# Optimization experiments

Measured on AMD Instinct MI355X. Metric: run time of the kernel, lower is better.

Reference implementation:

```python
import jax, jax.numpy as jnp
import numpy as np
import math

N = 100000   # outputSize (memory bank rows)
D = 128      # inputSize (feature dim)
B = 128      # batch size
K = 4096     # number of negatives per sample
T = 0.07     # temperature
MOMENTUM = 0.5


def setup_inputs() -> dict:
    key = jax.random.key(0)
    k1, k2, k3, k4, k5 = jax.random.split(key, 5)
    stdv = 1.0 / math.sqrt(D / 3.0)
    # l2-normalized features, as produced by the encoder in contrastive setups
    v1 = jax.random.normal(k1, (B, D), dtype=jnp.float32)
    v1 = v1 / jnp.linalg.norm(v1, axis=1, keepdims=True)
    v2 = jax.random.normal(k2, (B, D), dtype=jnp.float32)
    v2 = v2 / jnp.linalg.norm(v2, axis=1, keepdims=True)
    idx = jax.random.randint(k3, (B, K + 1), 0, N, dtype=jnp.int32)  # pos+neg bank rows
    y = jnp.arange(B, dtype=jnp.int32)  # distinct positive slots (first-visit behavior)
    # memory buffers initialized U(-stdv, stdv), as in torch.rand*2*stdv - stdv
    memory_v1 = jax.random.uniform(k4, (N, D), dtype=jnp.float32, minval=-stdv, maxval=stdv)
    memory_v2 = jax.random.uniform(k5, (N, D), dtype=jnp.float32, minval=-stdv, maxval=stdv)
    return {"v1": v1, "v2": v2, "idx": idx, "y": y,
            "memory_v1": memory_v1, "memory_v2": memory_v2}


def reference(v1, v2, idx, y, memory_v1, memory_v2):
    n_out = memory_v1.shape[0]
    # gather K+1 rows per sample (detached in the original -> stop_gradient)
    w1 = jax.lax.stop_gradient(memory_v1[idx])  # [B, K+1, D]
    w2 = jax.lax.stop_gradient(memory_v2[idx])  # [B, K+1, D]
    # batched vector-matrix product + exp/T
    out_v2 = jnp.exp(jnp.einsum('bkd,bd->bk', w1, v2) / T)  # [B, K+1]
    out_v1 = jnp.exp(jnp.einsum('bkd,bd->bk', w2, v1) / T)  # [B, K+1]
    # normalization constants (first-call Z computation: mean * outputSize)
    Z_v1 = jax.lax.stop_gradient(out_v1.mean()) * n_out
    Z_v2 = jax.lax.stop_gradient(out_v2.mean()) * n_out
    out_v1 = out_v1 / Z_v1
    out_v2 = out_v2 / Z_v2
    # momentum-blended normalize-and-scatter memory update (no_grad in torch)
    upd1 = MOMENTUM * memory_v1[y] + (1.0 - MOMENTUM) * v1  # [B, D]
    upd1 = upd1 / jnp.linalg.norm(upd1, axis=1, keepdims=True)
    new_memory_v1 = memory_v1.at[y].set(upd1)
    upd2 = MOMENTUM * memory_v2[y] + (1.0 - MOMENTUM) * v2
    upd2 = upd2 / jnp.linalg.norm(upd2, axis=1, keepdims=True)
    new_memory_v2 = memory_v2.at[y].set(upd2)
    return out_v1, out_v2, new_memory_v1, new_memory_v2
```

## Files before the change

### kernel.cpp

```cpp
#include <hip/hip_runtime.h>
#include <math.h>

constexpr int N_ROWS = 100000;
constexpr int D      = 128;
constexpr int B      = 128;
constexpr int KP1    = 4097;
constexpr int TOTAL_PAIRS = B * KP1;
constexpr float INV_T = 1.0f / 0.07f;
constexpr int N4 = N_ROWS * (D / 4);

constexpr int RPB  = 40;
constexpr int NB   = N_ROWS / RPB;
constexpr int PADR = 33;

constexpr size_t WS_BCNT   = 64;
constexpr size_t WS_BSTART = WS_BCNT + (size_t)NB * 16 * 4;
constexpr size_t WS_PLIST  = WS_BSTART + (size_t)(NB + 4) * 4;
constexpr size_t WS_NEEDED = WS_PLIST + (size_t)TOTAL_PAIRS * 4;
constexpr size_t WS_ZERO_BYTES = WS_BSTART;

typedef float fvec4 __attribute__((ext_vector_type(4)));

__device__ __forceinline__ float dot4(float4 a, float4 b) {
    return a.x * b.x + a.y * b.y + a.z * b.z + a.w * b.w;
}
__device__ __forceinline__ float red32(float v) {
    #pragma unroll
    for (int off = 16; off >= 1; off >>= 1) v += __shfl_xor(v, off);
    return v;
}

__global__ __launch_bounds__(256) void hist_kernel(
    const int* __restrict__ idx, int* __restrict__ bcnt) {
    int stride = gridDim.x * 256;
    for (int p = blockIdx.x * 256 + threadIdx.x; p < TOTAL_PAIRS; p += stride) {
        int bkt = idx[p] / RPB;
        atomicAdd(&bcnt[bkt * 16], 1);
    }
}

__global__ __launch_bounds__(1024) void scan_kernel(
    int* __restrict__ bcnt, int* __restrict__ bstart) {
    __shared__ int ssum[1024];
    const int t = threadIdx.x;
    const int b0 = 3 * t;
    int c0 = (b0     < NB) ? bcnt[(b0    ) * 16] : 0;
    int c1 = (b0 + 1 < NB) ? bcnt[(b0 + 1) * 16] : 0;
    int c2 = (b0 + 2 < NB) ? bcnt[(b0 + 2) * 16] : 0;
    int local = c0 + c1 + c2;
    ssum[t] = local;
    __syncthreads();
    for (int off = 1; off < 1024; off <<= 1) {
        int v = (t >= off) ? ssum[t - off] : 0;
        __syncthreads();
        ssum[t] += v;
        __syncthreads();
    }
    int excl = ssum[t] - local;
    if (b0     < NB) { bstart[b0]     = excl;           bcnt[(b0    ) * 16] = excl; }
    if (b0 + 1 < NB) { bstart[b0 + 1] = excl + c0;      bcnt[(b0 + 1) * 16] = excl + c0; }
    if (b0 + 2 < NB) { bstart[b0 + 2] = excl + c0 + c1; bcnt[(b0 + 2) * 16] = excl + c0 + c1; }
    if (t == 1023) bstart[NB] = ssum[1023];
}

__global__ __launch_bounds__(256) void scatter_kernel(
    const int* __restrict__ idx, int* __restrict__ bcnt,
    unsigned* __restrict__ plist) {
    int stride = gridDim.x * 256;
    for (int p = blockIdx.x * 256 + threadIdx.x; p < TOTAL_PAIRS; p += stride) {
        int r   = idx[p];
        int bkt = r / RPB;
        int lr  = r - bkt * RPB;
        int pos = atomicAdd(&bcnt[bkt * 16], 1);
        plist[pos] = (unsigned)p | ((unsigned)lr << 20);
    }
}

__global__ __launch_bounds__(256) void fused_kernel(
    const float* __restrict__ v1, const float* __restrict__ v2,
    const float* __restrict__ mem1, const float* __restrict__ mem2,
    const int* __restrict__ bstart, const unsigned* __restrict__ plist,
    float* __restrict__ out, float* __restrict__ sums,
    float* __restrict__ o1, float* __restrict__ o2)
{
    __shared__ float4 sm1[RPB * PADR];
    __shared__ float4 sm2[RPB * PADR];
    __shared__ float sz1[4], sz2[4];

    const int bid = blockIdx.x;
    const int tid = threadIdx.x;
    const int r0  = bid * RPB;

    const float4* __restrict__ M1 = (const float4*)mem1;
    const float4* __restrict__ M2 = (const float4*)mem2;
    const float4* __restrict__ V1 = (const float4*)v1;
    const float4* __restrict__ V2 = (const float4*)v2;
    fvec4* __restrict__ d1 = (fvec4*)o1;
    fvec4* __restrict__ d2 = (fvec4*)o2;

    for (int i = tid; i < RPB * 32; i += 256) {
        int lr = i >> 5, c = i & 31;
        size_t gi = (size_t)(r0 + lr) * 32 + c;
        float4 x1 = M1[gi];
        float4 x2 = M2[gi];
        sm1[lr * PADR + c] = x1;
        sm2[lr * PADR + c] = x2;
        fvec4 y1 = {x1.x, x1.y, x1.z, x1.w};
        fvec4 y2 = {x2.x, x2.y, x2.z, x2.w};
        __builtin_nontemporal_store(y1, &d1[gi]);
        __builtin_nontemporal_store(y2, &d2[gi]);
    }
    __syncthreads();

    const int team = tid >> 3;
    const int sub  = tid & 7;
    const int qend = bstart[bid + 1];
    float az1 = 0.0f, az2 = 0.0f;

    for (int q = bstart[bid] + team; q < qend; q += 32) {
        unsigned v = plist[q];
        int p  = (int)(v & 0xFFFFFu);
        int lr = (int)(v >> 20);
        int b  = p / KP1;

        const float4* __restrict__ w1 = &sm1[lr * PADR];
        const float4* __restrict__ w2 = &sm2[lr * PADR];
        float a = 0.0f, bb = 0.0f;
        #pragma unroll
        for (int i = 0; i < 4; ++i) {
            int c = sub + 8 * i;
            float4 vv1 = V1[b * 32 + c];
            float4 vv2 = V2[b * 32 + c];
            float4 x2  = w2[c];
            float4 x1  = w1[c];
            a  += dot4(x2, vv1);
            bb += dot4(x1, vv2);
        }
        #pragma unroll
        for (int off = 4; off >= 1; off >>= 1) {
            a  += __shfl_xor(a,  off);
            bb += __shfl_xor(bb, off);
        }
        float eA = __expf(a  * INV_T);
        float eB = __expf(bb * INV_T);
        az1 += eA;
        az2 += eB;
        if (sub < 2) out[(sub ? TOTAL_PAIRS : 0) + p] = sub ? eB : eA;
    }

    #pragma unroll
    for (int off = 32; off >= 1; off >>= 1) {
        az1 += __shfl_xor(az1, off);
        az2 += __shfl_xor(az2, off);
    }
    if ((tid & 63) == 0) { sz1[tid >> 6] = az1; sz2[tid >> 6] = az2; }
    __syncthreads();
    if (tid == 0) {
        float t1 = (sz1[0] + sz1[1] + sz1[2] + sz1[3]) * 0.125f;
        float t2 = (sz2[0] + sz2[1] + sz2[2] + sz2[3]) * 0.125f;
        atomicAdd(&sums[0], t1);
        atomicAdd(&sums[1], t2);
    }
}

__global__ __launch_bounds__(256) void finish_kernel(
    float* __restrict__ out, const float* __restrict__ sums,
    const float* __restrict__ v1, const float* __restrict__ v2,
    const int* __restrict__ y,
    const float* __restrict__ mem1, const float* __restrict__ mem2,
    float* __restrict__ o1, float* __restrict__ o2)
{
    if (blockIdx.x < 2 * B && threadIdx.x < 64) {
        int b    = blockIdx.x & (B - 1);
        int bank = blockIdx.x >> 7;
        int lane = threadIdx.x;
        const float2* __restrict__ m = (const float2*)(bank ? mem2 : mem1);
        const float2* __restrict__ v = (const float2*)(bank ? v2 : v1);
        float2* __restrict__ o       = (float2*)(bank ? o2 : o1);
        int row = y[b];
        float2 mv = m[(size_t)row * 64 + lane];
        float2 vv = v[b * 64 + lane];
        float2 u;
        u.x = 0.5f * mv.x + 0.5f * vv.x;
        u.y = 0.5f * mv.y + 0.5f * vv.y;
        float ss = u.x * u.x + u.y * u.y;
        #pragma unroll
        for (int off = 32; off >= 1; off >>= 1) ss += __shfl_xor(ss, off);
        float inv = 1.0f / sqrtf(ss);
        float2 r; r.x = u.x * inv; r.y = u.y * inv;
        o[(size_t)row * 64 + lane] = r;
    }

    float sc1 = (float)((double)TOTAL_PAIRS / ((double)sums[0] * (double)N_ROWS));
    float sc2 = (float)((double)TOTAL_PAIRS / ((double)sums[1] * (double)N_ROWS));
    int stride = gridDim.x * blockDim.x;
    for (int i = blockIdx.x * blockDim.x + threadIdx.x; i < 2 * TOTAL_PAIRS;
         i += stride) {
        out[i] *= (i < TOTAL_PAIRS) ? sc1 : sc2;
    }
}

__global__ void init_ws_kernel(float* ws) {
    if (threadIdx.x < 2) ws[threadIdx.x] = 0.0f;
}

__global__ __launch_bounds__(256) void score_kernel(
    const float* __restrict__ v1, const float* __restrict__ v2,
    const int* __restrict__ idx,
    const float* __restrict__ mem1, const float* __restrict__ mem2,
    float* __restrict__ out, float* __restrict__ sums)
{
    __shared__ alignas(16) int s_idx[260];
    __shared__ float s1[8], s2[8];
    const int sid   = blockIdx.x;
    const int tid   = threadIdx.x;
    const int l     = tid & 31;
    const int grp   = tid >> 5;
    const int b     = sid >> 4;
    const int chunk = sid & 15;
    const int cnt   = (chunk == 15) ? 257 : 256;
    const int ibase = b * KP1 + chunk * 256;
    for (int t = tid; t < cnt; t += 256) s_idx[t] = idx[ibase + t];
    __syncthreads();
    const float4* __restrict__ m1 = (const float4*)mem1;
    const float4* __restrict__ m2 = (const float4*)mem2;
    const float4 a1 = ((const float4*)v1)[b * 32 + l];
    const float4 a2 = ((const float4*)v2)[b * 32 + l];
    const int lk = grp * 32, pbase = ibase + lk;
    float acc1 = 0.0f, acc2 = 0.0f;
    for (int u = 0; u < 32; u += 4) {
        const int4 rr = *(const int4*)&s_idx[lk + u];
        float4 wA0 = m2[(size_t)rr.x * 32 + l], wB0 = m1[(size_t)rr.x * 32 + l];
        float4 wA1 = m2[(size_t)rr.y * 32 + l], wB1 = m1[(size_t)rr.y * 32 + l];
        float4 wA2 = m2[(size_t)rr.z * 32 + l], wB2 = m1[(size_t)rr.z * 32 + l];
        float4 wA3 = m2[(size_t)rr.w * 32 + l], wB3 = m1[(size_t)rr.w * 32 + l];
        float eA0 = __expf(red32(dot4(wA0, a1)) * INV_T);
        float eB0 = __expf(red32(dot4(wB0, a2)) * INV_T);
        float eA1 = __expf(red32(dot4(wA1, a1)) * INV_T);
        float eB1 = __expf(red32(dot4(wB1, a2)) * INV_T);
        float eA2 = __expf(red32(dot4(wA2, a1)) * INV_T);
        float eB2 = __expf(red32(dot4(wB2, a2)) * INV_T);
        float eA3 = __expf(red32(dot4(wA3, a1)) * INV_T);
        float eB3 = __expf(red32(dot4(wB3, a2)) * INV_T);
        acc1 += (eA0 + eA1) + (eA2 + eA3);
        acc2 += (eB0 + eB1) + (eB2 + eB3);
        float sa = (l & 1) ? eA1 : eA0, sb = (l & 1) ? eA3 : eA2;
        float evA = (l & 2) ? sb : sa;
        float sc = (l & 1) ? eB1 : eB0, sd = (l & 1) ? eB3 : eB2;
        float evB = (l & 2) ? sd : sc;
        int p = pbase + u;
        if (l < 4)      out[p + l] = evA;
        else if (l < 8) out[TOTAL_PAIRS + p + (l - 4)] = evB;
    }
    if (chunk == 15 && grp == 7) {
        int r = s_idx[256];
        float4 wA = m2[(size_t)r * 32 + l], wB = m1[(size_t)r * 32 + l];
        float eA = __expf(red32(dot4(wA, a1)) * INV_T);
        float eB = __expf(red32(dot4(wB, a2)) * INV_T);
        acc1 += eA; acc2 += eB;
        if (l == 0) {
            out[b * KP1 + 4096] = eA;
            out[TOTAL_PAIRS + b * KP1 + 4096] = eB;
        }
    }
    if (l == 0) { s1[grp] = acc1; s2[grp] = acc2; }
    __syncthreads();
    if (tid == 0) {
        float t1 = 0.0f, t2 = 0.0f;
        #pragma unroll
        for (int i = 0; i < 8; ++i) { t1 += s1[i]; t2 += s2[i]; }
        atomicAdd(&sums[0], t1);
        atomicAdd(&sums[1], t2);
    }
}

__global__ __launch_bounds__(256) void copy_scale_kernel(
    const float* __restrict__ mem1, const float* __restrict__ mem2,
    float* __restrict__ o1, float* __restrict__ o2,
    float* __restrict__ out, const float* __restrict__ sums)
{
    const fvec4* __restrict__ m1 = (const fvec4*)mem1;
    const fvec4* __restrict__ m2 = (const fvec4*)mem2;
    fvec4* __restrict__ d1 = (fvec4*)o1;
    fvec4* __restrict__ d2 = (fvec4*)o2;
    int tid = blockIdx.x * 256 + threadIdx.x;
    int stride = gridDim.x * 256;
    for (int i = tid; i < N4; i += stride) {
        fvec4 x1 = m1[i], x2 = m2[i];
        __builtin_nontemporal_store(x1, &d1[i]);
        __builtin_nontemporal_store(x2, &d2[i]);
    }
    float sc1 = (float)((double)TOTAL_PAIRS / ((double)sums[0] * (double)N_ROWS));
    float sc2 = (float)((double)TOTAL_PAIRS / ((double)sums[1] * (double)N_ROWS));
    for (int i = tid; i < 2 * TOTAL_PAIRS; i += stride) {
        out[i] *= (i < TOTAL_PAIRS) ? sc1 : sc2;
    }
}

__global__ void rowupd_kernel(
    const float* __restrict__ v1, const float* __restrict__ v2,
    const int* __restrict__ y,
    const float* __restrict__ mem1, const float* __restrict__ mem2,
    float* __restrict__ o1, float* __restrict__ o2)
{
    int b    = blockIdx.x & (B - 1);
    int bank = blockIdx.x >> 7;
    int lane = threadIdx.x;
    const float2* __restrict__ m = (const float2*)(bank ? mem2 : mem1);
    const float2* __restrict__ v = (const float2*)(bank ? v2 : v1);
    float2* __restrict__ o       = (float2*)(bank ? o2 : o1);
    int row = y[b];
    float2 mv = m[(size_t)row * 64 + lane];
    float2 vv = v[b * 64 + lane];
    float2 u;
    u.x = 0.5f * mv.x + 0.5f * vv.x;
    u.y = 0.5f * mv.y + 0.5f * vv.y;
    float ss = u.x * u.x + u.y * u.y;
    #pragma unroll
    for (int off = 32; off >= 1; off >>= 1) ss += __shfl_xor(ss, off);
    float inv = 1.0f / sqrtf(ss);
    float2 r; r.x = u.x * inv; r.y = u.y * inv;
    o[(size_t)row * 64 + lane] = r;
}

extern "C" void kernel_launch(void* const* d_in, const int* in_sizes, int n_in,
                              void* d_out, int out_size, void* d_ws, size_t ws_size,
                              hipStream_t stream) {
    const float* v1   = (const float*)d_in[0];
    const float* v2   = (const float*)d_in[1];
    const int*   idx  = (const int*)d_in[2];
    const int*   y    = (const int*)d_in[3];
    const float* mem1 = (const float*)d_in[4];
    const float* mem2 = (const float*)d_in[5];

    float* out = (float*)d_out;
    float* out_mem1 = out + 2 * (size_t)TOTAL_PAIRS;
    float* out_mem2 = out_mem1 + (size_t)N_ROWS * D;
    char*  ws   = (char*)d_ws;
    float* sums = (float*)d_ws;

    if (ws_size >= WS_NEEDED) {
        int*      bcnt   = (int*)(ws + WS_BCNT);
        int*      bstart = (int*)(ws + WS_BSTART);
        unsigned* plist  = (unsigned*)(ws + WS_PLIST);

        hipMemsetAsync(ws, 0, WS_ZERO_BYTES, stream);
        hist_kernel<<<512, 256, 0, stream>>>(idx, bcnt);
        scan_kernel<<<1, 1024, 0, stream>>>(bcnt, bstart);
        scatter_kernel<<<512, 256, 0, stream>>>(idx, bcnt, plist);
        fused_kernel<<<NB, 256, 0, stream>>>(
            v1, v2, mem1, mem2, bstart, plist,
            out, sums, out_mem1, out_mem2);
        finish_kernel<<<1024, 256, 0, stream>>>(
            out, sums, v1, v2, y, mem1, mem2, out_mem1, out_mem2);
    } else {
        init_ws_kernel<<<1, 64, 0, stream>>>(sums);
        score_kernel<<<2048, 256, 0, stream>>>(
            v1, v2, idx, mem1, mem2, out, sums);
        copy_scale_kernel<<<2048, 256, 0, stream>>>(
            mem1, mem2, out_mem1, out_mem2, out, sums);
        rowupd_kernel<<<2 * B, 64, 0, stream>>>(
            v1, v2, y, mem1, mem2, out_mem1, out_mem2);
    }
}
```

Before: 314.6 us.

## Shrink bucket to 16 rows, use shift indexing and pack batch id into plist

Lowers rows per bucket and fused block from 40 to 16, so bucket index and local row come from a shift and a mask instead of division. The histogram counters are no longer padded to one per 16 ints, the scan kernel handles 7 buckets per thread, and the batch index is packed into the high bits of each plist entry so the fused kernel skips a division by KP1. The smaller blocks mean far more blocks and more contention on the bucket atomics now that they are densely packed. The workspace offsets are hardcoded constants that have to match the new NB.

```diff
diff --git a/kernel.cpp b/kernel.cpp
--- a/kernel.cpp
+++ b/kernel.cpp
@@ -9,13 +9,13 @@
 constexpr float INV_T = 1.0f / 0.07f;
 constexpr int N4 = N_ROWS * (D / 4);
 
-constexpr int RPB  = 40;
+constexpr int RPB  = 16;
 constexpr int NB   = N_ROWS / RPB;
 constexpr int PADR = 33;
 
 constexpr size_t WS_BCNT   = 64;
-constexpr size_t WS_BSTART = WS_BCNT + (size_t)NB * 16 * 4;
-constexpr size_t WS_PLIST  = WS_BSTART + (size_t)(NB + 4) * 4;
+constexpr size_t WS_BSTART = 25088;
+constexpr size_t WS_PLIST  = 50112;
 constexpr size_t WS_NEEDED = WS_PLIST + (size_t)TOTAL_PAIRS * 4;
 constexpr size_t WS_ZERO_BYTES = WS_BSTART;
 
@@ -33,21 +33,22 @@
 __global__ __launch_bounds__(256) void hist_kernel(
     const int* __restrict__ idx, int* __restrict__ bcnt) {
     int stride = gridDim.x * 256;
-    for (int p = blockIdx.x * 256 + threadIdx.x; p < TOTAL_PAIRS; p += stride) {
-        int bkt = idx[p] / RPB;
-        atomicAdd(&bcnt[bkt * 16], 1);
-    }
+    for (int p = blockIdx.x * 256 + threadIdx.x; p < TOTAL_PAIRS; p += stride)
+        atomicAdd(&bcnt[idx[p] >> 4], 1);
 }
 
 __global__ __launch_bounds__(1024) void scan_kernel(
     int* __restrict__ bcnt, int* __restrict__ bstart) {
     __shared__ int ssum[1024];
-    const int t = threadIdx.x;
-    const int b0 = 3 * t;
-    int c0 = (b0     < NB) ? bcnt[(b0    ) * 16] : 0;
-    int c1 = (b0 + 1 < NB) ? bcnt[(b0 + 1) * 16] : 0;
-    int c2 = (b0 + 2 < NB) ? bcnt[(b0 + 2) * 16] : 0;
-    int local = c0 + c1 + c2;
+    const int t  = threadIdx.x;
+    const int j0 = t * 7;
+    int c[7];
+    int local = 0;
+    #pragma unroll
+    for (int i = 0; i < 7; ++i) {
+        c[i] = (j0 + i < NB) ? bcnt[j0 + i] : 0;
+        local += c[i];
+    }
     ssum[t] = local;
     __syncthreads();
     for (int off = 1; off < 1024; off <<= 1) {
@@ -56,10 +57,12 @@
         ssum[t] += v;
         __syncthreads();
     }
-    int excl = ssum[t] - local;
-    if (b0     < NB) { bstart[b0]     = excl;           bcnt[(b0    ) * 16] = excl; }
-    if (b0 + 1 < NB) { bstart[b0 + 1] = excl + c0;      bcnt[(b0 + 1) * 16] = excl + c0; }
-    if (b0 + 2 < NB) { bstart[b0 + 2] = excl + c0 + c1; bcnt[(b0 + 2) * 16] = excl + c0 + c1; }
+    int run = ssum[t] - local;
+    #pragma unroll
+    for (int i = 0; i < 7; ++i) {
+        if (j0 + i < NB) { bstart[j0 + i] = run; bcnt[j0 + i] = run; }
+        run += c[i];
+    }
     if (t == 1023) bstart[NB] = ssum[1023];
 }
 
@@ -69,10 +72,11 @@
     int stride = gridDim.x * 256;
     for (int p = blockIdx.x * 256 + threadIdx.x; p < TOTAL_PAIRS; p += stride) {
         int r   = idx[p];
-        int bkt = r / RPB;
-        int lr  = r - bkt * RPB;
-        int pos = atomicAdd(&bcnt[bkt * 16], 1);
-        plist[pos] = (unsigned)p | ((unsigned)lr << 20);
+        int bkt = r >> 4;
+        int lr  = r & 15;
+        int b   = p / KP1;
+        int pos = atomicAdd(&bcnt[bkt], 1);
+        plist[pos] = (unsigned)p | ((unsigned)lr << 20) | ((unsigned)b << 24);
     }
 }
 
@@ -98,7 +102,9 @@
     fvec4* __restrict__ d1 = (fvec4*)o1;
     fvec4* __restrict__ d2 = (fvec4*)o2;
 
-    for (int i = tid; i < RPB * 32; i += 256) {
+    #pragma unroll
+    for (int it = 0; it < 2; ++it) {
+        int i  = it * 256 + tid;
         int lr = i >> 5, c = i & 31;
         size_t gi = (size_t)(r0 + lr) * 32 + c;
         float4 x1 = M1[gi];
@@ -120,8 +126,8 @@
     for (int q = bstart[bid] + team; q < qend; q += 32) {
         unsigned v = plist[q];
         int p  = (int)(v & 0xFFFFFu);
-        int lr = (int)(v >> 20);
-        int b  = p / KP1;
+        int lr = (int)((v >> 20) & 15u);
+        int b  = (int)(v >> 24);
 
         const float4* __restrict__ w1 = &sm1[lr * PADR];
         const float4* __restrict__ w2 = &sm2[lr * PADR];
```

After: 381.4 us. 1.21x slower.

## Replace histogram+scan bucketing with fixed-capacity buckets and overflow fallback

Applied to the files above, without the earlier changes.

Drops the histogram and prefix-scan kernels by scattering pair indices into fixed-capacity per-bucket slots, with rare overflow pairs handled by a small fallback kernel. The bank copy is moved into interleaved dedicated blocks of the fused kernel, the bucket list is staged in shared memory, and each team processes two pairs per iteration for more ILP. This removes a pass over idx and two launches, at the cost of a fixed capacity assumption and a serial overflow path.

```diff
diff --git a/kernel.cpp b/kernel.cpp
--- a/kernel.cpp
+++ b/kernel.cpp
@@ -11,13 +11,16 @@
 
 constexpr int RPB  = 40;
 constexpr int NB   = N_ROWS / RPB;
+constexpr int CAP  = 284;
 constexpr int PADR = 33;
+constexpr int OVF_MAX = 4096;
 
 constexpr size_t WS_BCNT   = 64;
-constexpr size_t WS_BSTART = WS_BCNT + (size_t)NB * 16 * 4;
-constexpr size_t WS_PLIST  = WS_BSTART + (size_t)(NB + 4) * 4;
-constexpr size_t WS_NEEDED = WS_PLIST + (size_t)TOTAL_PAIRS * 4;
-constexpr size_t WS_ZERO_BYTES = WS_BSTART;
+constexpr size_t WS_OVFC   = 10064;
+constexpr size_t WS_OVF    = 10080;
+constexpr size_t WS_PLIST  = 26496;
+constexpr size_t WS_NEEDED = WS_PLIST + (size_t)NB * CAP * 4;
+constexpr size_t WS_ZERO_BYTES = WS_OVF;
 
 typedef float fvec4 __attribute__((ext_vector_type(4)));
 
@@ -30,122 +33,127 @@
     return v;
 }
 
-__global__ __launch_bounds__(256) void hist_kernel(
-    const int* __restrict__ idx, int* __restrict__ bcnt) {
-    int stride = gridDim.x * 256;
-    for (int p = blockIdx.x * 256 + threadIdx.x; p < TOTAL_PAIRS; p += stride) {
-        int bkt = idx[p] / RPB;
-        atomicAdd(&bcnt[bkt * 16], 1);
-    }
-}
-
-__global__ __launch_bounds__(1024) void scan_kernel(
-    int* __restrict__ bcnt, int* __restrict__ bstart) {
-    __shared__ int ssum[1024];
-    const int t = threadIdx.x;
-    const int b0 = 3 * t;
-    int c0 = (b0     < NB) ? bcnt[(b0    ) * 16] : 0;
-    int c1 = (b0 + 1 < NB) ? bcnt[(b0 + 1) * 16] : 0;
-    int c2 = (b0 + 2 < NB) ? bcnt[(b0 + 2) * 16] : 0;
-    int local = c0 + c1 + c2;
-    ssum[t] = local;
-    __syncthreads();
-    for (int off = 1; off < 1024; off <<= 1) {
-        int v = (t >= off) ? ssum[t - off] : 0;
-        __syncthreads();
-        ssum[t] += v;
-        __syncthreads();
-    }
-    int excl = ssum[t] - local;
-    if (b0     < NB) { bstart[b0]     = excl;           bcnt[(b0    ) * 16] = excl; }
-    if (b0 + 1 < NB) { bstart[b0 + 1] = excl + c0;      bcnt[(b0 + 1) * 16] = excl + c0; }
-    if (b0 + 2 < NB) { bstart[b0 + 2] = excl + c0 + c1; bcnt[(b0 + 2) * 16] = excl + c0 + c1; }
-    if (t == 1023) bstart[NB] = ssum[1023];
-}
-
 __global__ __launch_bounds__(256) void scatter_kernel(
     const int* __restrict__ idx, int* __restrict__ bcnt,
+    int* __restrict__ ovfc, int* __restrict__ ovf,
     unsigned* __restrict__ plist) {
     int stride = gridDim.x * 256;
     for (int p = blockIdx.x * 256 + threadIdx.x; p < TOTAL_PAIRS; p += stride) {
         int r   = idx[p];
         int bkt = r / RPB;
         int lr  = r - bkt * RPB;
-        int pos = atomicAdd(&bcnt[bkt * 16], 1);
-        plist[pos] = (unsigned)p | ((unsigned)lr << 20);
-    }
-}
-
-__global__ __launch_bounds__(256) void fused_kernel(
+        int pos = atomicAdd(&bcnt[bkt], 1);
+        if (pos < CAP) {
+            plist[bkt * CAP + pos] = (unsigned)p | ((unsigned)lr << 20);
+        } else {
+            int o = atomicAdd(ovfc, 1);
+            if (o < OVF_MAX) ovf[o] = p;
+        }
+    }
+}
+
+__global__ __launch_bounds__(256, 4) void fused_mega(
     const float* __restrict__ v1, const float* __restrict__ v2,
     const float* __restrict__ mem1, const float* __restrict__ mem2,
-    const int* __restrict__ bstart, const unsigned* __restrict__ plist,
+    const int* __restrict__ bcnt, const unsigned* __restrict__ plist,
     float* __restrict__ out, float* __restrict__ sums,
     float* __restrict__ o1, float* __restrict__ o2)
 {
+    if (blockIdx.x & 1) {
+        int cid = blockIdx.x >> 1;
+        const fvec4* __restrict__ m1 = (const fvec4*)mem1;
+        const fvec4* __restrict__ m2 = (const fvec4*)mem2;
+        fvec4* __restrict__ d1 = (fvec4*)o1;
+        fvec4* __restrict__ d2 = (fvec4*)o2;
+        int t = cid * 256 + threadIdx.x;
+        int stride = NB * 256;
+        for (int i = t; i < N4; i += stride) {
+            fvec4 x1 = m1[i];
+            fvec4 x2 = m2[i];
+            __builtin_nontemporal_store(x1, &d1[i]);
+            __builtin_nontemporal_store(x2, &d2[i]);
+        }
+        return;
+    }
+
     __shared__ float4 sm1[RPB * PADR];
     __shared__ float4 sm2[RPB * PADR];
+    __shared__ unsigned s_pl[CAP];
     __shared__ float sz1[4], sz2[4];
 
-    const int bid = blockIdx.x;
+    const int sid = blockIdx.x >> 1;
     const int tid = threadIdx.x;
-    const int r0  = bid * RPB;
+    const int r0  = sid * RPB;
 
     const float4* __restrict__ M1 = (const float4*)mem1;
     const float4* __restrict__ M2 = (const float4*)mem2;
     const float4* __restrict__ V1 = (const float4*)v1;
     const float4* __restrict__ V2 = (const float4*)v2;
-    fvec4* __restrict__ d1 = (fvec4*)o1;
-    fvec4* __restrict__ d2 = (fvec4*)o2;
 
     for (int i = tid; i < RPB * 32; i += 256) {
         int lr = i >> 5, c = i & 31;
         size_t gi = (size_t)(r0 + lr) * 32 + c;
-        float4 x1 = M1[gi];
-        float4 x2 = M2[gi];
-        sm1[lr * PADR + c] = x1;
-        sm2[lr * PADR + c] = x2;
-        fvec4 y1 = {x1.x, x1.y, x1.z, x1.w};
-        fvec4 y2 = {x2.x, x2.y, x2.z, x2.w};
-        __builtin_nontemporal_store(y1, &d1[gi]);
-        __builtin_nontemporal_store(y2, &d2[gi]);
-    }
+        sm1[lr * PADR + c] = M1[gi];
+        sm2[lr * PADR + c] = M2[gi];
+    }
+    int cnt = bcnt[sid];
+    if (cnt > CAP) cnt = CAP;
+    for (int t = tid; t < cnt; t += 256) s_pl[t] = plist[sid * CAP + t];
     __syncthreads();
 
     const int team = tid >> 3;
     const int sub  = tid & 7;
-    const int qend = bstart[bid + 1];
     float az1 = 0.0f, az2 = 0.0f;
 
-    for (int q = bstart[bid] + team; q < qend; q += 32) {
-        unsigned v = plist[q];
-        int p  = (int)(v & 0xFFFFFu);
-        int lr = (int)(v >> 20);
-        int b  = p / KP1;
-
-        const float4* __restrict__ w1 = &sm1[lr * PADR];
-        const float4* __restrict__ w2 = &sm2[lr * PADR];
-        float a = 0.0f, bb = 0.0f;
+    for (int q = team; q < cnt; q += 64) {
+        unsigned e0 = s_pl[q];
+        int q1 = q + 32;
+        bool have1 = (q1 < cnt);
+        unsigned e1 = have1 ? s_pl[q1] : e0;
+
+        int p0 = (int)(e0 & 0xFFFFFu), lr0 = (int)(e0 >> 20);
+        int p1 = (int)(e1 & 0xFFFFFu), lr1 = (int)(e1 >> 20);
+        int b0 = p0 / KP1;
+        int b1 = p1 / KP1;
+
+        const float4* __restrict__ w10 = &sm1[lr0 * PADR];
+        const float4* __restrict__ w20 = &sm2[lr0 * PADR];
+        const float4* __restrict__ w11 = &sm1[lr1 * PADR];
+        const float4* __restrict__ w21 = &sm2[lr1 * PADR];
+
+        float a0 = 0.0f, c0 = 0.0f, a1 = 0.0f, c1 = 0.0f;
         #pragma unroll
         for (int i = 0; i < 4; ++i) {
             int c = sub + 8 * i;
-            float4 vv1 = V1[b * 32 + c];
-            float4 vv2 = V2[b * 32 + c];
-            float4 x2  = w2[c];
-            float4 x1  = w1[c];
-            a  += dot4(x2, vv1);
-            bb += dot4(x1, vv2);
+            float4 va0 = V1[b0 * 32 + c];
+            float4 vb0 = V2[b0 * 32 + c];
+            float4 va1 = V1[b1 * 32 + c];
+            float4 vb1 = V2[b1 * 32 + c];
+            float4 x20 = w20[c], x10 = w10[c];
+            float4 x21 = w21[c], x11 = w11[c];
+            a0 += dot4(x20, va0);
+            c0 += dot4(x10, vb0);
+            a1 += dot4(x21, va1);
+            c1 += dot4(x11, vb1);
         }
         #pragma unroll
         for (int off = 4; off >= 1; off >>= 1) {
-            a  += __shfl_xor(a,  off);
-            bb += __shfl_xor(bb, off);
-        }
-        float eA = __expf(a  * INV_T);
-        float eB = __expf(bb * INV_T);
-        az1 += eA;
-        az2 += eB;
-        if (sub < 2) out[(sub ? TOTAL_PAIRS : 0) + p] = sub ? eB : eA;
+            a0 += __shfl_xor(a0, off);
+            c0 += __shfl_xor(c0, off);
+            a1 += __shfl_xor(a1, off);
+            c1 += __shfl_xor(c1, off);
+        }
+        float eA0 = __expf(a0 * INV_T), eB0 = __expf(c0 * INV_T);
+        float eA1 = __expf(a1 * INV_T), eB1 = __expf(c1 * INV_T);
+
+        az1 += eA0; az2 += eB0;
+        if (sub == 0) out[p0] = eA0;
+        else if (sub == 1) out[TOTAL_PAIRS + p0] = eB0;
+        if (have1) {
+            az1 += eA1; az2 += eB1;
+            if (sub == 0) out[p1] = eA1;
+            else if (sub == 1) out[TOTAL_PAIRS + p1] = eB1;
+        }
     }
 
     #pragma unroll
@@ -160,6 +168,40 @@
         float t2 = (sz2[0] + sz2[1] + sz2[2] + sz2[3]) * 0.125f;
         atomicAdd(&sums[0], t1);
         atomicAdd(&sums[1], t2);
+    }
+}
+
+__global__ void ovf_kernel(
+    const int* __restrict__ idx,
+    const float* __restrict__ v1, const float* __restrict__ v2,
+    const float* __restrict__ mem1, const float* __restrict__ mem2,
+    const int* __restrict__ ovfc, const int* __restrict__ ovf,
+    float* __restrict__ out, float* __restrict__ sums)
+{
+    int n = *ovfc;
+    if (n > OVF_MAX) n = OVF_MAX;
+    const float4* __restrict__ M1 = (const float4*)mem1;
+    const float4* __restrict__ M2 = (const float4*)mem2;
+    const float4* __restrict__ V1 = (const float4*)v1;
+    const float4* __restrict__ V2 = (const float4*)v2;
+    for (int i = threadIdx.x; i < n; i += 256) {
+        int p = ovf[i];
+        int r = idx[p];
+        int b = p / KP1;
+        float a = 0.0f, c = 0.0f;
+        for (int j = 0; j < 32; ++j) {
+            float4 w1 = M1[(size_t)r * 32 + j];
+            float4 w2 = M2[(size_t)r * 32 + j];
+            float4 x1 = V1[b * 32 + j];
+            float4 x2 = V2[b * 32 + j];
+            a += dot4(w2, x1);
+            c += dot4(w1, x2);
+        }
+        float eA = __expf(a * INV_T), eB = __expf(c * INV_T);
+        out[p] = eA;
+        out[TOTAL_PAIRS + p] = eB;
+        atomicAdd(&sums[0], eA);
+        atomicAdd(&sums[1], eB);
     }
 }
 
@@ -340,17 +382,18 @@
     float* sums = (float*)d_ws;
 
     if (ws_size >= WS_NEEDED) {
-        int*      bcnt   = (int*)(ws + WS_BCNT);
-        int*      bstart = (int*)(ws + WS_BSTART);
-        unsigned* plist  = (unsigned*)(ws + WS_PLIST);
+        int*      bcnt  = (int*)(ws + WS_BCNT);
+        int*      ovfc  = (int*)(ws + WS_OVFC);
+        int*      ovf   = (int*)(ws + WS_OVF);
+        unsigned* plist = (unsigned*)(ws + WS_PLIST);
 
         hipMemsetAsync(ws, 0, WS_ZERO_BYTES, stream);
-        hist_kernel<<<512, 256, 0, stream>>>(idx, bcnt);
-        scan_kernel<<<1, 1024, 0, stream>>>(bcnt, bstart);
-        scatter_kernel<<<512, 256, 0, stream>>>(idx, bcnt, plist);
-        fused_kernel<<<NB, 256, 0, stream>>>(
-            v1, v2, mem1, mem2, bstart, plist,
+        scatter_kernel<<<512, 256, 0, stream>>>(idx, bcnt, ovfc, ovf, plist);
+        fused_mega<<<2 * NB, 256, 0, stream>>>(
+            v1, v2, mem1, mem2, bcnt, plist,
             out, sums, out_mem1, out_mem2);
+        ovf_kernel<<<1, 256, 0, stream>>>(
+            idx, v1, v2, mem1, mem2, ovfc, ovf, out, sums);
         finish_kernel<<<1024, 256, 0, stream>>>(
             out, sums, v1, v2, y, mem1, mem2, out_mem1, out_mem2);
     } else {
```

After: 304.6 us. -3.2%, faster.
